# Performance work log

Hardware: AMD Instinct MI355X
Metric: run time of the kernel (lower is better)

## Reference

```python
import jax, jax.numpy as jnp
import numpy as np

TOP_K = 2

def setup_inputs() -> dict:
    key = jax.random.key(0)
    ks = jax.random.split(key, 8)
    B, T, C, E, I, S = 1, 2048, 2048, 8, 1408, 2816
    s = 0.02  # weight scale for numerical stability
    return {
        "x": jax.random.normal(ks[0], (B, T, C), jnp.float32),
        "gate_w": jax.random.normal(ks[1], (E, C), jnp.float32) * s,
        "w1": jax.random.normal(ks[2], (E, I, C), jnp.float32) * s,
        "w3": jax.random.normal(ks[3], (E, I, C), jnp.float32) * s,
        "w2": jax.random.normal(ks[4], (E, C, I), jnp.float32) * s,
        "sw1": jax.random.normal(ks[5], (S, C), jnp.float32) * s,
        "sw3": jax.random.normal(ks[6], (S, C), jnp.float32) * s,
        "sw2": jax.random.normal(ks[7], (C, S), jnp.float32) * s,
    }

def reference(x, gate_w, w1, w3, w2, sw1, sw3, sw2):
    B, T, C = x.shape
    E = gate_w.shape[0]
    xf = x.reshape(-1, C)                      # [N, C]
    N = xf.shape[0]
    # --- routing: top-k of raw logits, softmax over the k selected logits ---
    logits = xf @ gate_w.T                     # [N, E]
    pv, idx = jax.lax.top_k(logits, TOP_K)     # [N, K]
    pv = jax.nn.softmax(pv.astype(jnp.float32), axis=-1).astype(x.dtype)
    # token-expert combine weights (sum of probs per expert, scatter of top-k)
    tew = jnp.zeros((N, E), x.dtype).at[jnp.arange(N)[:, None], idx].add(pv)
    # --- experts (SwiGLU), computed densely over all experts and masked by tew ---
    h = jax.nn.silu(jnp.einsum('nc,eic->nei', xf, w1)) * jnp.einsum('nc,eic->nei', xf, w3)
    eo = jnp.einsum('nei,eci->nec', h, w2)     # [N, E, C]
    y = jnp.einsum('nec,ne->nc', eo, tew).reshape(B, T, C)
    # --- shared expert on the residual input ---
    sh = (jax.nn.silu(x @ sw1.T) * (x @ sw3.T)) @ sw2.T
    return y + sh
```

## Files before the change

kernel.cpp:

```cpp
#include <hip/hip_runtime.h>

#define DEVI __device__ __forceinline__

typedef __attribute__((ext_vector_type(4))) float f32x4;
typedef __attribute__((ext_vector_type(8))) short bf16x8;

static constexpr int NT = 2048;
static constexpr int CD = 2048;
static constexpr int NE = 8;
static constexpr int ID = 1408;
static constexpr int SD = 2816;
static constexpr int ROWS = 2 * NT;
static constexpr int ROWS_PAD = ROWS + 256;

DEVI unsigned short f2bf(float f) {
  unsigned u = __builtin_bit_cast(unsigned, f);
  u += 0x7fff + ((u >> 16) & 1);
  return (unsigned short)(u >> 16);
}
DEVI float bf2f(unsigned short s) { return __builtin_bit_cast(float, (unsigned)s << 16); }
DEVI float silu_f(float z) { return z / (1.f + __expf(-z)); }

DEVI void gll16(const void* g, void* l) {
  __builtin_amdgcn_global_load_lds((__attribute__((address_space(1))) void*)(void*)g,
                                   (__attribute__((address_space(3))) void*)l, 16, 0, 0);
}

DEVI void bar_sched() {
  __builtin_amdgcn_s_barrier();
  __builtin_amdgcn_sched_barrier(0);
}
DEVI void sched0() { __builtin_amdgcn_sched_barrier(0); }
DEVI void wait_vm0() { asm volatile("s_waitcnt vmcnt(0)" ::: "memory"); }
DEVI void wait_lgk0() { asm volatile("s_waitcnt lgkmcnt(0)" ::: "memory"); }

DEVI int swz8(int bid, int nwg) {
  constexpr int CH = 8, G = 64;
  int nfull = nwg - (nwg % G);
  if (bid >= nfull) return bid;
  int c = bid / G, r = bid % G;
  return c * G + (r % 8) * CH + (r / 8);
}

__global__ __launch_bounds__(256) void k_cvt(const float* __restrict__ s,
                                             unsigned short* __restrict__ d, int n8)
{
  int i = blockIdx.x * 256 + threadIdx.x;
  int stride = gridDim.x * 256;
  for (; i < n8; i += stride) {
    float4 a = ((const float4*)s)[2 * i];
    float4 b = ((const float4*)s)[2 * i + 1];
    ushort4 p0 = make_ushort4(f2bf(a.x), f2bf(a.y), f2bf(a.z), f2bf(a.w));
    ushort4 p1 = make_ushort4(f2bf(b.x), f2bf(b.y), f2bf(b.z), f2bf(b.w));
    ((ushort4*)d)[2 * i]     = p0;
    ((ushort4*)d)[2 * i + 1] = p1;
  }
}

__global__ __launch_bounds__(64) void k_router(const float* __restrict__ x,
    const float* __restrict__ gw, int* __restrict__ counts,
    int* __restrict__ eidx, int* __restrict__ posn, float* __restrict__ probs)
{
  const int n = blockIdx.x;
  const int lane = threadIdx.x;
  const float4* xr = (const float4*)(x + (size_t)n * CD);
  float acc[NE];
#pragma unroll
  for (int e = 0; e < NE; ++e) acc[e] = 0.f;
  for (int i = lane; i < CD / 4; i += 64) {
    float4 xv = xr[i];
#pragma unroll
    for (int e = 0; e < NE; ++e) {
      float4 gv = ((const float4*)(gw + (size_t)e * CD))[i];
      acc[e] += xv.x * gv.x + xv.y * gv.y + xv.z * gv.z + xv.w * gv.w;
    }
  }
#pragma unroll
  for (int e = 0; e < NE; ++e) {
    float v = acc[e];
#pragma unroll
    for (int off = 32; off > 0; off >>= 1) v += __shfl_down(v, off);
    acc[e] = v;
  }
  if (lane == 0) {
    int b0 = 0; float m0 = acc[0];
#pragma unroll
    for (int e = 1; e < NE; ++e) if (acc[e] > m0) { m0 = acc[e]; b0 = e; }
    int b1 = -1; float m1 = 0.f;
#pragma unroll
    for (int e = 0; e < NE; ++e) {
      if (e == b0) continue;
      if (b1 < 0 || acc[e] > m1) { m1 = acc[e]; b1 = e; }
    }
    float d = __expf(m1 - m0);
    float inv = 1.f / (1.f + d);
    eidx[2 * n] = b0; eidx[2 * n + 1] = b1;
    probs[2 * n] = inv; probs[2 * n + 1] = d * inv;
    posn[2 * n] = atomicAdd(&counts[b0], 1);
    posn[2 * n + 1] = atomicAdd(&counts[b1], 1);
  }
}

__global__ void k_scan(const int* __restrict__ counts, int* __restrict__ bases) {
  if (threadIdx.x == 0) {
    int s = 0;
    for (int e = 0; e < NE; ++e) { bases[e] = s; s += counts[e]; }
  }
}

__global__ __launch_bounds__(256) void k_build(const int* __restrict__ eidx,
    const int* __restrict__ posn, const int* __restrict__ bases,
    int* __restrict__ rows_of, int* __restrict__ row2tok)
{
  int n = blockIdx.x * 256 + threadIdx.x;
  if (n >= NT) return;
#pragma unroll
  for (int k = 0; k < 2; ++k) {
    int e = eidx[2 * n + k];
    int row = bases[e] + posn[2 * n + k];
    rows_of[2 * n + k] = row;
    row2tok[row] = n;
  }
}

__global__ __launch_bounds__(512, 2) void k_up(
    const unsigned short* __restrict__ xb,
    const unsigned short* __restrict__ w1b, const unsigned short* __restrict__ w3b,
    const unsigned short* __restrict__ sw1b, const unsigned short* __restrict__ sw3b,
    unsigned short* __restrict__ h, unsigned short* __restrict__ hs,
    const int* __restrict__ counts, const int* __restrict__ bases,
    const int* __restrict__ row2tok)
{
  extern __shared__ char sm[];
  constexpr int NSH = (NT / 256) * (SD / 128);
  constexpr int NWG = NSH + NE * (ID / 128) * (NT / 256);
  constexpr int NSTEP = CD / 64;

  int lin = swz8((int)blockIdx.x, NWG);
  int cls, mx, pn, e = 0;
  if (lin < NSH) { cls = 0; mx = lin % 8; pn = lin / 8; }
  else { cls = 1; int r = lin - NSH; mx = r % 8; r /= 8; pn = r % 11; e = r / 11; }

  int M = NT, baserow = 0;
  if (cls) { M = counts[e]; if (mx * 256 >= M) return; baserow = bases[e]; }
  const int m0 = mx * 256, n0 = pn * 128;

  const unsigned short* B1 = cls ? w1b + ((size_t)e * ID + n0) * CD : sw1b + (size_t)n0 * CD;
  const unsigned short* B3 = cls ? w3b + ((size_t)e * ID + n0) * CD : sw3b + (size_t)n0 * CD;

  const int tid = threadIdx.x, l = tid & 63, w = tid >> 6;
  const int wr = w >> 2, wn = w & 3;
  const int slot = ((tid & 7) ^ ((tid >> 3) & 7)) * 16;

  const char* aP[4];
#pragma unroll
  for (int t = 0; t < 4; ++t) {
    int r = t * 64 + (tid >> 3);
    const unsigned short* rb;
    if (cls) {
      int grow = m0 + r; int gr = grow < M ? grow : 0;
      rb = xb + (size_t)row2tok[baserow + gr] * CD;
    } else {
      rb = xb + (size_t)(m0 + r) * CD;
    }
    aP[t] = (const char*)rb + slot;
  }
  const char* bP1[2]; const char* bP3[2];
#pragma unroll
  for (int t = 0; t < 2; ++t) {
    int r = t * 64 + (tid >> 3);
    bP1[t] = (const char*)(B1 + (size_t)r * CD) + slot;
    bP3[t] = (const char*)(B3 + (size_t)r * CD) + slot;
  }

  f32x4 acc1[8][2], acc3[8][2];
#pragma unroll
  for (int m = 0; m < 8; ++m)
#pragma unroll
    for (int n = 0; n < 2; ++n) {
      acc1[m][n] = {0.f, 0.f, 0.f, 0.f};
      acc3[m][n] = {0.f, 0.f, 0.f, 0.f};
    }

  const int lrow = l & 15, lkg = l >> 4, l7 = l & 7;

  auto stage_first = [&](char* base, size_t kb) {
#pragma unroll
    for (int t = 0; t < 4; ++t) gll16(aP[t] + kb, base + t * 8192 + tid * 16);
  };
  auto stage_second = [&](char* base, size_t kb) {
    char* sB1 = base + 32768; char* sB3 = base + 49152;
#pragma unroll
    for (int t = 0; t < 2; ++t) {
      gll16(bP1[t] + kb, sB1 + t * 8192 + tid * 16);
      gll16(bP3[t] + kb, sB3 + t * 8192 + tid * 16);
    }
  };
  auto ldq = [&](bf16x8* fa, bf16x8* fb1, bf16x8* fb3, const char* cur, int mh, int kk) {
    const char* sA = cur; const char* sB1 = cur + 32768; const char* sB3 = cur + 49152;
    const int ao = ((kk * 4 + lkg) ^ l7) * 16;
#pragma unroll
    for (int m = 0; m < 4; ++m)
      fa[m] = *(const bf16x8*)(sA + (wr * 128 + mh * 64 + m * 16 + lrow) * 128 + ao);
#pragma unroll
    for (int n = 0; n < 2; ++n) {
      fb1[n] = *(const bf16x8*)(sB1 + (wn * 32 + n * 16 + lrow) * 128 + ao);
      fb3[n] = *(const bf16x8*)(sB3 + (wn * 32 + n * 16 + lrow) * 128 + ao);
    }
  };
  auto mmq = [&](const bf16x8* fa, const bf16x8* fb1, const bf16x8* fb3, int mh) {
    __builtin_amdgcn_s_setprio(1);
#pragma unroll
    for (int n = 0; n < 2; ++n)
#pragma unroll
      for (int m = 0; m < 4; ++m) {
        acc1[mh * 4 + m][n] = __builtin_amdgcn_mfma_f32_16x16x32_bf16(fa[m], fb1[n], acc1[mh * 4 + m][n], 0, 0, 0);
        acc3[mh * 4 + m][n] = __builtin_amdgcn_mfma_f32_16x16x32_bf16(fa[m], fb3[n], acc3[mh * 4 + m][n], 0, 0, 0);
      }
    __builtin_amdgcn_s_setprio(0);
  };

  stage_first(sm, 0);
  stage_second(sm, 0);
  wait_vm0(); bar_sched();

  bf16x8 Xa[4], Xb1[2], Xb3[2], Ya[4], Yb1[2], Yb3[2];

  for (int t = 0; t < NSTEP; ++t) {
    char* cur = sm + (size_t)(t & 1) * 65536;
    char* nxt = sm + (size_t)((t + 1) & 1) * 65536;
    size_t kb = (size_t)(t + 1) * 128;
    ldq(Xa, Xb1, Xb3, cur, 0, 0);
    sched0();
    if (t + 1 < NSTEP) stage_first(nxt, kb);
    ldq(Ya, Yb1, Yb3, cur, 1, 0);
    mmq(Xa, Xb1, Xb3, 0);
    sched0();
    if (t + 1 < NSTEP) stage_second(nxt, kb);
    ldq(Xa, Xb1, Xb3, cur, 0, 1);
    mmq(Ya, Yb1, Yb3, 1);
    sched0();
    ldq(Ya, Yb1, Yb3, cur, 1, 1);
    mmq(Xa, Xb1, Xb3, 0);
    sched0();
    mmq(Ya, Yb1, Yb3, 1);
    sched0();
    wait_vm0(); wait_lgk0();
    bar_sched();
  }

#pragma unroll
  for (int m = 0; m < 8; ++m) {
    int rb_ = m0 + wr * 128 + m * 16 + lkg * 4;
#pragma unroll
    for (int j = 0; j < 4; ++j) {
      int grow = rb_ + j;
      if (cls && grow >= M) continue;
#pragma unroll
      for (int n = 0; n < 2; ++n) {
        int gcol = n0 + wn * 32 + n * 16 + lrow;
        float hh = silu_f(acc1[m][n][j]) * acc3[m][n][j];
        if (cls) h[(size_t)(baserow + grow) * ID + gcol] = f2bf(hh);
        else     hs[(size_t)grow * SD + gcol] = f2bf(hh);
      }
    }
  }
}

__global__ __launch_bounds__(512, 2) void k_down(
    const unsigned short* __restrict__ h, const unsigned short* __restrict__ hs,
    const unsigned short* __restrict__ w2b, const unsigned short* __restrict__ sw2b,
    unsigned short* __restrict__ eo, float* __restrict__ y,
    const int* __restrict__ counts, const int* __restrict__ bases)
{
  extern __shared__ char sm[];
  constexpr int NRT = NE * (CD / 256) * (NT / 256);
  constexpr int NWG = NRT + (CD / 256) * (NT / 256);

  int lin = swz8((int)blockIdx.x, NWG);
  int cls, mx, pn, e = 0;
  if (lin < NRT) { cls = 1; mx = lin % 8; int r = lin / 8; pn = r % 8; e = r / 8; }
  else { cls = 0; int r = lin - NRT; mx = r % 8; pn = r / 8; }

  int M = NT, baserow = 0;
  if (cls) { M = counts[e]; if (mx * 256 >= M) return; baserow = bases[e]; }
  const int m0 = mx * 256, n0 = pn * 256;
  const int KD_ = cls ? ID : SD;
  const int nstep = KD_ / 64;

  const unsigned short* B = cls ? w2b + ((size_t)e * CD + n0) * ID : sw2b + (size_t)n0 * SD;

  const int tid = threadIdx.x, l = tid & 63, w = tid >> 6;
  const int wr = w >> 2, wn = w & 3;
  const int slot = ((tid & 7) ^ ((tid >> 3) & 7)) * 16;

  const char* aP[4]; const char* bP[4];
#pragma unroll
  for (int t = 0; t < 4; ++t) {
    int r = t * 64 + (tid >> 3);
    const unsigned short* rb = cls ? h + (size_t)(baserow + m0 + r) * ID
                                   : hs + (size_t)(m0 + r) * SD;
    aP[t] = (const char*)rb + slot;
    bP[t] = (const char*)(B + (size_t)r * KD_) + slot;
  }

  f32x4 acc[8][4];
#pragma unroll
  for (int m = 0; m < 8; ++m)
#pragma unroll
    for (int n = 0; n < 4; ++n) acc[m][n] = {0.f, 0.f, 0.f, 0.f};

  const int lrow = l & 15, lkg = l >> 4, l7 = l & 7;

  auto stage_first = [&](char* base, size_t kb) {
#pragma unroll
    for (int t = 0; t < 4; ++t) gll16(aP[t] + kb, base + t * 8192 + tid * 16);
  };
  auto stage_second = [&](char* base, size_t kb) {
    char* sB = base + 32768;
#pragma unroll
    for (int t = 0; t < 4; ++t) gll16(bP[t] + kb, sB + t * 8192 + tid * 16);
  };
  auto ldq = [&](bf16x8* fa, bf16x8* fb, const char* cur, int mh, int kk) {
    const char* sA = cur; const char* sB = cur + 32768;
    const int ao = ((kk * 4 + lkg) ^ l7) * 16;
#pragma unroll
    for (int m = 0; m < 4; ++m)
      fa[m] = *(const bf16x8*)(sA + (wr * 128 + mh * 64 + m * 16 + lrow) * 128 + ao);
#pragma unroll
    for (int n = 0; n < 4; ++n)
      fb[n] = *(const bf16x8*)(sB + (wn * 64 + n * 16 + lrow) * 128 + ao);
  };
  auto mmq = [&](const bf16x8* fa, const bf16x8* fb, int mh) {
    __builtin_amdgcn_s_setprio(1);
#pragma unroll
    for (int n = 0; n < 4; ++n)
#pragma unroll
      for (int m = 0; m < 4; ++m)
        acc[mh * 4 + m][n] = __builtin_amdgcn_mfma_f32_16x16x32_bf16(fa[m], fb[n], acc[mh * 4 + m][n], 0, 0, 0);
    __builtin_amdgcn_s_setprio(0);
  };

  stage_first(sm, 0);
  stage_second(sm, 0);
  wait_vm0(); bar_sched();

  bf16x8 Xa[4], Xb[4], Ya[4], Yb[4];

  for (int t = 0; t < nstep; ++t) {
    char* cur = sm + (size_t)(t & 1) * 65536;
    char* nxt = sm + (size_t)((t + 1) & 1) * 65536;
    size_t kb = (size_t)(t + 1) * 128;
    ldq(Xa, Xb, cur, 0, 0);
    sched0();
    if (t + 1 < nstep) stage_first(nxt, kb);
    ldq(Ya, Yb, cur, 1, 0);
    mmq(Xa, Xb, 0);
    sched0();
    if (t + 1 < nstep) stage_second(nxt, kb);
    ldq(Xa, Xb, cur, 0, 1);
    mmq(Ya, Yb, 1);
    sched0();
    ldq(Ya, Yb, cur, 1, 1);
    mmq(Xa, Xb, 0);
    sched0();
    mmq(Ya, Yb, 1);
    sched0();
    wait_vm0(); wait_lgk0();
    bar_sched();
  }

#pragma unroll
  for (int m = 0; m < 8; ++m) {
    int rb_ = m0 + wr * 128 + m * 16 + lkg * 4;
#pragma unroll
    for (int j = 0; j < 4; ++j) {
      int grow = rb_ + j;
      if (cls && grow >= M) continue;
#pragma unroll
      for (int n = 0; n < 4; ++n) {
        int gcol = n0 + wn * 64 + n * 16 + lrow;
        float v = acc[m][n][j];
        if (cls) eo[(size_t)(baserow + grow) * CD + gcol] = f2bf(v);
        else     y[(size_t)grow * CD + gcol] = v;
      }
    }
  }
}

__global__ __launch_bounds__(256) void k_combine(float* __restrict__ y,
    const unsigned short* __restrict__ eo, const int* __restrict__ rows_of,
    const float* __restrict__ probs)
{
  const int n = blockIdx.x;
  const int c = threadIdx.x * 8;
  const int r0 = rows_of[2 * n], r1 = rows_of[2 * n + 1];
  const float p0 = probs[2 * n], p1 = probs[2 * n + 1];
  bf16x8 e0 = *(const bf16x8*)(eo + (size_t)r0 * CD + c);
  bf16x8 e1 = *(const bf16x8*)(eo + (size_t)r1 * CD + c);
  float* yp = y + (size_t)n * CD + c;
  float4 y0 = *(float4*)yp, y1 = *(float4*)(yp + 4);
  y0.x += p0 * bf2f((unsigned short)e0[0]) + p1 * bf2f((unsigned short)e1[0]);
  y0.y += p0 * bf2f((unsigned short)e0[1]) + p1 * bf2f((unsigned short)e1[1]);
  y0.z += p0 * bf2f((unsigned short)e0[2]) + p1 * bf2f((unsigned short)e1[2]);
  y0.w += p0 * bf2f((unsigned short)e0[3]) + p1 * bf2f((unsigned short)e1[3]);
  y1.x += p0 * bf2f((unsigned short)e0[4]) + p1 * bf2f((unsigned short)e1[4]);
  y1.y += p0 * bf2f((unsigned short)e0[5]) + p1 * bf2f((unsigned short)e1[5]);
  y1.z += p0 * bf2f((unsigned short)e0[6]) + p1 * bf2f((unsigned short)e1[6]);
  y1.w += p0 * bf2f((unsigned short)e0[7]) + p1 * bf2f((unsigned short)e1[7]);
  *(float4*)yp = y0; *(float4*)(yp + 4) = y1;
}

extern "C" void kernel_launch(void* const* d_in, const int* in_sizes, int n_in,
                              void* d_out, int out_size, void* d_ws, size_t ws_size,
                              hipStream_t stream)
{
  const float* x   = (const float*)d_in[0];
  const float* gw  = (const float*)d_in[1];
  const float* w1  = (const float*)d_in[2];
  const float* w3  = (const float*)d_in[3];
  const float* w2  = (const float*)d_in[4];
  const float* sw1 = (const float*)d_in[5];
  const float* sw3 = (const float*)d_in[6];
  const float* sw2 = (const float*)d_in[7];
  float* y = (float*)d_out;

  char* p = (char*)d_ws;
  auto alloc = [&](size_t b) { char* r = p; p += (b + 255) & ~(size_t)255; return r; };
  int*   counts  = (int*)alloc(NE * 4);
  int*   bases   = (int*)alloc(NE * 4);
  int*   eidx    = (int*)alloc((size_t)NT * 2 * 4);
  int*   posn    = (int*)alloc((size_t)NT * 2 * 4);
  float* probs   = (float*)alloc((size_t)NT * 2 * 4);
  int*   rows_of = (int*)alloc((size_t)NT * 2 * 4);
  int*   row2tok = (int*)alloc((size_t)ROWS * 4);
  unsigned short* xb   = (unsigned short*)alloc((size_t)NT * CD * 2);
  unsigned short* w1b  = (unsigned short*)alloc((size_t)NE * ID * CD * 2);
  unsigned short* w3b  = (unsigned short*)alloc((size_t)NE * ID * CD * 2);
  unsigned short* w2b  = (unsigned short*)alloc((size_t)NE * CD * ID * 2);
  unsigned short* sw1b = (unsigned short*)alloc((size_t)SD * CD * 2);
  unsigned short* sw3b = (unsigned short*)alloc((size_t)SD * CD * 2);
  unsigned short* sw2b = (unsigned short*)alloc((size_t)CD * SD * 2);
  unsigned short* h    = (unsigned short*)alloc((size_t)ROWS_PAD * ID * 2);
  unsigned short* eo   = (unsigned short*)alloc((size_t)ROWS_PAD * CD * 2);
  unsigned short* hs   = (unsigned short*)alloc((size_t)NT * SD * 2);

  hipFuncSetAttribute((const void*)k_up,   hipFuncAttributeMaxDynamicSharedMemorySize, 131072);
  hipFuncSetAttribute((const void*)k_down, hipFuncAttributeMaxDynamicSharedMemorySize, 131072);

  hipMemsetAsync(counts, 0, NE * 4, stream);

  auto cvt = [&](const float* s, unsigned short* d, size_t n) {
    int n8 = (int)(n / 8);
    int grid = (n8 + 255) / 256; if (grid > 2048) grid = 2048;
    k_cvt<<<grid, 256, 0, stream>>>(s, d, n8);
  };
  cvt(x,   xb,   (size_t)NT * CD);
  cvt(w1,  w1b,  (size_t)NE * ID * CD);
  cvt(w3,  w3b,  (size_t)NE * ID * CD);
  cvt(w2,  w2b,  (size_t)NE * CD * ID);
  cvt(sw1, sw1b, (size_t)SD * CD);
  cvt(sw3, sw3b, (size_t)SD * CD);
  cvt(sw2, sw2b, (size_t)CD * SD);

  k_router<<<NT, 64, 0, stream>>>(x, gw, counts, eidx, posn, probs);
  k_scan<<<1, 64, 0, stream>>>(counts, bases);
  k_build<<<NT / 256, 256, 0, stream>>>(eidx, posn, bases, rows_of, row2tok);

  {
    constexpr int NWG = (NT / 256) * (SD / 128) + NE * (ID / 128) * (NT / 256);
    k_up<<<NWG, 512, 131072, stream>>>(xb, w1b, w3b, sw1b, sw3b, h, hs,
                                       counts, bases, row2tok);
  }
  {
    constexpr int NWG = NE * (CD / 256) * (NT / 256) + (CD / 256) * (NT / 256);
    k_down<<<NWG, 512, 131072, stream>>>(h, hs, w2b, sw2b, eo, y, counts, bases);
  }
  k_combine<<<NT, 256, 0, stream>>>(y, eo, rows_of, probs);
}
```

Baseline: 437.1 us.

## Shrink GEMM tiles and use triple-buffered LDS prefetch two steps ahead

```diff
diff --git a/kernel.cpp b/kernel.cpp
--- a/kernel.cpp
+++ b/kernel.cpp
@@ -12,6 +12,7 @@
 static constexpr int SD = 2816;
 static constexpr int ROWS = 2 * NT;
 static constexpr int ROWS_PAD = ROWS + 256;
+static constexpr int BUFSZ = 49152;
 
 DEVI unsigned short f2bf(float f) {
   unsigned u = __builtin_bit_cast(unsigned, f);
@@ -31,8 +32,8 @@
   __builtin_amdgcn_sched_barrier(0);
 }
 DEVI void sched0() { __builtin_amdgcn_sched_barrier(0); }
+DEVI void wait_vm6() { asm volatile("s_waitcnt vmcnt(6)" ::: "memory"); }
 DEVI void wait_vm0() { asm volatile("s_waitcnt vmcnt(0)" ::: "memory"); }
-DEVI void wait_lgk0() { asm volatile("s_waitcnt lgkmcnt(0)" ::: "memory"); }
 
 DEVI int swz8(int bid, int nwg) {
   constexpr int CH = 8, G = 64;
@@ -132,18 +133,18 @@
     const int* __restrict__ row2tok)
 {
   extern __shared__ char sm[];
-  constexpr int NSH = (NT / 256) * (SD / 128);
-  constexpr int NWG = NSH + NE * (ID / 128) * (NT / 256);
+  constexpr int NSH = (NT / 128) * (SD / 128);
+  constexpr int NWG = NSH + NE * (ID / 128) * (NT / 128);
   constexpr int NSTEP = CD / 64;
 
   int lin = swz8((int)blockIdx.x, NWG);
   int cls, mx, pn, e = 0;
-  if (lin < NSH) { cls = 0; mx = lin % 8; pn = lin / 8; }
-  else { cls = 1; int r = lin - NSH; mx = r % 8; r /= 8; pn = r % 11; e = r / 11; }
+  if (lin < NSH) { cls = 0; mx = lin % 16; pn = lin / 16; }
+  else { cls = 1; int r = lin - NSH; mx = r % 16; r /= 16; pn = r % 11; e = r / 11; }
 
   int M = NT, baserow = 0;
-  if (cls) { M = counts[e]; if (mx * 256 >= M) return; baserow = bases[e]; }
-  const int m0 = mx * 256, n0 = pn * 128;
+  if (cls) { M = counts[e]; if (mx * 128 >= M) return; baserow = bases[e]; }
+  const int m0 = mx * 128, n0 = pn * 128;
 
   const unsigned short* B1 = cls ? w1b + ((size_t)e * ID + n0) * CD : sw1b + (size_t)n0 * CD;
   const unsigned short* B3 = cls ? w3b + ((size_t)e * ID + n0) * CD : sw3b + (size_t)n0 * CD;
@@ -152,9 +153,9 @@
   const int wr = w >> 2, wn = w & 3;
   const int slot = ((tid & 7) ^ ((tid >> 3) & 7)) * 16;
 
-  const char* aP[4];
-#pragma unroll
-  for (int t = 0; t < 4; ++t) {
+  const char* aP[2];
+#pragma unroll
+  for (int t = 0; t < 2; ++t) {
     int r = t * 64 + (tid >> 3);
     const unsigned short* rb;
     if (cls) {
@@ -173,9 +174,9 @@
     bP3[t] = (const char*)(B3 + (size_t)r * CD) + slot;
   }
 
-  f32x4 acc1[8][2], acc3[8][2];
-#pragma unroll
-  for (int m = 0; m < 8; ++m)
+  f32x4 acc1[4][2], acc3[4][2];
+#pragma unroll
+  for (int m = 0; m < 4; ++m)
 #pragma unroll
     for (int n = 0; n < 2; ++n) {
       acc1[m][n] = {0.f, 0.f, 0.f, 0.f};
@@ -184,24 +185,24 @@
 
   const int lrow = l & 15, lkg = l >> 4, l7 = l & 7;
 
-  auto stage_first = [&](char* base, size_t kb) {
-#pragma unroll
-    for (int t = 0; t < 4; ++t) gll16(aP[t] + kb, base + t * 8192 + tid * 16);
-  };
-  auto stage_second = [&](char* base, size_t kb) {
-    char* sB1 = base + 32768; char* sB3 = base + 49152;
-#pragma unroll
-    for (int t = 0; t < 2; ++t) {
-      gll16(bP1[t] + kb, sB1 + t * 8192 + tid * 16);
-      gll16(bP3[t] + kb, sB3 + t * 8192 + tid * 16);
-    }
+  auto stageA = [&](char* buf, size_t kb) {
+    gll16(aP[0] + kb, buf + tid * 16);
+    gll16(aP[1] + kb, buf + 8192 + tid * 16);
+  };
+  auto stageB1c = [&](char* buf, size_t kb) {
+    gll16(bP1[0] + kb, buf + 16384 + tid * 16);
+    gll16(bP1[1] + kb, buf + 24576 + tid * 16);
+  };
+  auto stageB3c = [&](char* buf, size_t kb) {
+    gll16(bP3[0] + kb, buf + 32768 + tid * 16);
+    gll16(bP3[1] + kb, buf + 40960 + tid * 16);
   };
   auto ldq = [&](bf16x8* fa, bf16x8* fb1, bf16x8* fb3, const char* cur, int mh, int kk) {
-    const char* sA = cur; const char* sB1 = cur + 32768; const char* sB3 = cur + 49152;
+    const char* sA = cur; const char* sB1 = cur + 16384; const char* sB3 = cur + 32768;
     const int ao = ((kk * 4 + lkg) ^ l7) * 16;
 #pragma unroll
-    for (int m = 0; m < 4; ++m)
-      fa[m] = *(const bf16x8*)(sA + (wr * 128 + mh * 64 + m * 16 + lrow) * 128 + ao);
+    for (int m = 0; m < 2; ++m)
+      fa[m] = *(const bf16x8*)(sA + (wr * 64 + mh * 32 + m * 16 + lrow) * 128 + ao);
 #pragma unroll
     for (int n = 0; n < 2; ++n) {
       fb1[n] = *(const bf16x8*)(sB1 + (wn * 32 + n * 16 + lrow) * 128 + ao);
@@ -213,45 +214,46 @@
 #pragma unroll
     for (int n = 0; n < 2; ++n)
 #pragma unroll
-      for (int m = 0; m < 4; ++m) {
-        acc1[mh * 4 + m][n] = __builtin_amdgcn_mfma_f32_16x16x32_bf16(fa[m], fb1[n], acc1[mh * 4 + m][n], 0, 0, 0);
-        acc3[mh * 4 + m][n] = __builtin_amdgcn_mfma_f32_16x16x32_bf16(fa[m], fb3[n], acc3[mh * 4 + m][n], 0, 0, 0);
+      for (int m = 0; m < 2; ++m) {
+        acc1[mh * 2 + m][n] = __builtin_amdgcn_mfma_f32_16x16x32_bf16(fa[m], fb1[n], acc1[mh * 2 + m][n], 0, 0, 0);
+        acc3[mh * 2 + m][n] = __builtin_amdgcn_mfma_f32_16x16x32_bf16(fa[m], fb3[n], acc3[mh * 2 + m][n], 0, 0, 0);
       }
     __builtin_amdgcn_s_setprio(0);
   };
 
-  stage_first(sm, 0);
-  stage_second(sm, 0);
-  wait_vm0(); bar_sched();
-
-  bf16x8 Xa[4], Xb1[2], Xb3[2], Ya[4], Yb1[2], Yb3[2];
+  stageA(sm, 0); stageB1c(sm, 0); stageB3c(sm, 0);
+  stageA(sm + BUFSZ, 128); stageB1c(sm + BUFSZ, 128); stageB3c(sm + BUFSZ, 128);
+
+  bf16x8 Xa[2], Xb1[2], Xb3[2], Ya[2], Yb1[2], Yb3[2];
 
   for (int t = 0; t < NSTEP; ++t) {
-    char* cur = sm + (size_t)(t & 1) * 65536;
-    char* nxt = sm + (size_t)((t + 1) & 1) * 65536;
-    size_t kb = (size_t)(t + 1) * 128;
+    if (t == NSTEP - 1) wait_vm0(); else wait_vm6();
+    bar_sched();
+    const char* cur = sm + (size_t)(t % 3) * BUFSZ;
+    char* nb = sm + (size_t)((t + 2) % 3) * BUFSZ;
+    const bool pf = (t + 2 < NSTEP);
+    const size_t kb = (size_t)(t + 2) * 128;
     ldq(Xa, Xb1, Xb3, cur, 0, 0);
     sched0();
-    if (t + 1 < NSTEP) stage_first(nxt, kb);
+    if (pf) stageA(nb, kb);
     ldq(Ya, Yb1, Yb3, cur, 1, 0);
     mmq(Xa, Xb1, Xb3, 0);
     sched0();
-    if (t + 1 < NSTEP) stage_second(nxt, kb);
+    if (pf) stageB1c(nb, kb);
     ldq(Xa, Xb1, Xb3, cur, 0, 1);
     mmq(Ya, Yb1, Yb3, 1);
     sched0();
+    if (pf) stageB3c(nb, kb);
     ldq(Ya, Yb1, Yb3, cur, 1, 1);
     mmq(Xa, Xb1, Xb3, 0);
     sched0();
     mmq(Ya, Yb1, Yb3, 1);
     sched0();
-    wait_vm0(); wait_lgk0();
-    bar_sched();
-  }
-
-#pragma unroll
-  for (int m = 0; m < 8; ++m) {
-    int rb_ = m0 + wr * 128 + m * 16 + lkg * 4;
+  }
+
+#pragma unroll
+  for (int m = 0; m < 4; ++m) {
+    int rb_ = m0 + wr * 64 + m * 16 + lkg * 4;
 #pragma unroll
     for (int j = 0; j < 4; ++j) {
       int grow = rb_ + j;
@@ -274,17 +276,17 @@
     const int* __restrict__ counts, const int* __restrict__ bases)
 {
   extern __shared__ char sm[];
-  constexpr int NRT = NE * (CD / 256) * (NT / 256);
-  constexpr int NWG = NRT + (CD / 256) * (NT / 256);
+  constexpr int NRT = NE * (CD / 128) * (NT / 256);
+  constexpr int NWG = NRT + (CD / 128) * (NT / 256);
 
   int lin = swz8((int)blockIdx.x, NWG);
   int cls, mx, pn, e = 0;
-  if (lin < NRT) { cls = 1; mx = lin % 8; int r = lin / 8; pn = r % 8; e = r / 8; }
+  if (lin < NRT) { cls = 1; mx = lin % 8; int r = lin / 8; pn = r % 16; e = r / 16; }
   else { cls = 0; int r = lin - NRT; mx = r % 8; pn = r / 8; }
 
   int M = NT, baserow = 0;
   if (cls) { M = counts[e]; if (mx * 256 >= M) return; baserow = bases[e]; }
-  const int m0 = mx * 256, n0 = pn * 256;
+  const int m0 = mx * 256, n0 = pn * 128;
   const int KD_ = cls ? ID : SD;
   const int nstep = KD_ / 64;
 
@@ -294,32 +296,39 @@
   const int wr = w >> 2, wn = w & 3;
   const int slot = ((tid & 7) ^ ((tid >> 3) & 7)) * 16;
 
-  const char* aP[4]; const char* bP[4];
+  const char* aP[4]; const char* bP[2];
 #pragma unroll
   for (int t = 0; t < 4; ++t) {
     int r = t * 64 + (tid >> 3);
     const unsigned short* rb = cls ? h + (size_t)(baserow + m0 + r) * ID
                                    : hs + (size_t)(m0 + r) * SD;
     aP[t] = (const char*)rb + slot;
+  }
+#pragma unroll
+  for (int t = 0; t < 2; ++t) {
+    int r = t * 64 + (tid >> 3);
     bP[t] = (const char*)(B + (size_t)r * KD_) + slot;
   }
 
-  f32x4 acc[8][4];
+  f32x4 acc[8][2];
 #pragma unroll
   for (int m = 0; m < 8; ++m)
 #pragma unroll
-    for (int n = 0; n < 4; ++n) acc[m][n] = {0.f, 0.f, 0.f, 0.f};
+    for (int n = 0; n < 2; ++n) acc[m][n] = {0.f, 0.f, 0.f, 0.f};
 
   const int lrow = l & 15, lkg = l >> 4, l7 = l & 7;
 
-  auto stage_first = [&](char* base, size_t kb) {
-#pragma unroll
-    for (int t = 0; t < 4; ++t) gll16(aP[t] + kb, base + t * 8192 + tid * 16);
-  };
-  auto stage_second = [&](char* base, size_t kb) {
-    char* sB = base + 32768;
-#pragma unroll
-    for (int t = 0; t < 4; ++t) gll16(bP[t] + kb, sB + t * 8192 + tid * 16);
+  auto stageA01 = [&](char* buf, size_t kb) {
+    gll16(aP[0] + kb, buf + tid * 16);
+    gll16(aP[1] + kb, buf + 8192 + tid * 16);
+  };
+  auto stageA23 = [&](char* buf, size_t kb) {
+    gll16(aP[2] + kb, buf + 16384 + tid * 16);
+    gll16(aP[3] + kb, buf + 24576 + tid * 16);
+  };
+  auto stageB = [&](char* buf, size_t kb) {
+    gll16(bP[0] + kb, buf + 32768 + tid * 16);
+    gll16(bP[1] + kb, buf + 40960 + tid * 16);
   };
   auto ldq = [&](bf16x8* fa, bf16x8* fb, const char* cur, int mh, int kk) {
     const char* sA = cur; const char* sB = cur + 32768;
@@ -328,46 +337,47 @@
     for (int m = 0; m < 4; ++m)
       fa[m] = *(const bf16x8*)(sA + (wr * 128 + mh * 64 + m * 16 + lrow) * 128 + ao);
 #pragma unroll
-    for (int n = 0; n < 4; ++n)
-      fb[n] = *(const bf16x8*)(sB + (wn * 64 + n * 16 + lrow) * 128 + ao);
+    for (int n = 0; n < 2; ++n)
+      fb[n] = *(const bf16x8*)(sB + (wn * 32 + n * 16 + lrow) * 128 + ao);
   };
   auto mmq = [&](const bf16x8* fa, const bf16x8* fb, int mh) {
     __builtin_amdgcn_s_setprio(1);
 #pragma unroll
-    for (int n = 0; n < 4; ++n)
+    for (int n = 0; n < 2; ++n)
 #pragma unroll
       for (int m = 0; m < 4; ++m)
         acc[mh * 4 + m][n] = __builtin_amdgcn_mfma_f32_16x16x32_bf16(fa[m], fb[n], acc[mh * 4 + m][n], 0, 0, 0);
     __builtin_amdgcn_s_setprio(0);
   };
 
-  stage_first(sm, 0);
-  stage_second(sm, 0);
-  wait_vm0(); bar_sched();
-
-  bf16x8 Xa[4], Xb[4], Ya[4], Yb[4];
+  stageA01(sm, 0); stageA23(sm, 0); stageB(sm, 0);
+  stageA01(sm + BUFSZ, 128); stageA23(sm + BUFSZ, 128); stageB(sm + BUFSZ, 128);
+
+  bf16x8 Xa[4], Xb[2], Ya[4], Yb[2];
 
   for (int t = 0; t < nstep; ++t) {
-    char* cur = sm + (size_t)(t & 1) * 65536;
-    char* nxt = sm + (size_t)((t + 1) & 1) * 65536;
-    size_t kb = (size_t)(t + 1) * 128;
+    if (t == nstep - 1) wait_vm0(); else wait_vm6();
+    bar_sched();
+    const char* cur = sm + (size_t)(t % 3) * BUFSZ;
+    char* nb = sm + (size_t)((t + 2) % 3) * BUFSZ;
+    const bool pf = (t + 2 < nstep);
+    const size_t kb = (size_t)(t + 2) * 128;
     ldq(Xa, Xb, cur, 0, 0);
     sched0();
-    if (t + 1 < nstep) stage_first(nxt, kb);
+    if (pf) stageA01(nb, kb);
     ldq(Ya, Yb, cur, 1, 0);
     mmq(Xa, Xb, 0);
     sched0();
-    if (t + 1 < nstep) stage_second(nxt, kb);
+    if (pf) stageA23(nb, kb);
     ldq(Xa, Xb, cur, 0, 1);
     mmq(Ya, Yb, 1);
     sched0();
+    if (pf) stageB(nb, kb);
     ldq(Ya, Yb, cur, 1, 1);
     mmq(Xa, Xb, 0);
     sched0();
     mmq(Ya, Yb, 1);
     sched0();
-    wait_vm0(); wait_lgk0();
-    bar_sched();
   }
 
 #pragma unroll
@@ -378,8 +388,8 @@
       int grow = rb_ + j;
       if (cls && grow >= M) continue;
 #pragma unroll
-      for (int n = 0; n < 4; ++n) {
-        int gcol = n0 + wn * 64 + n * 16 + lrow;
+      for (int n = 0; n < 2; ++n) {
+        int gcol = n0 + wn * 32 + n * 16 + lrow;
         float v = acc[m][n][j];
         if (cls) eo[(size_t)(baserow + grow) * CD + gcol] = f2bf(v);
         else     y[(size_t)grow * CD + gcol] = v;
@@ -445,8 +455,8 @@
   unsigned short* eo   = (unsigned short*)alloc((size_t)ROWS_PAD * CD * 2);
   unsigned short* hs   = (unsigned short*)alloc((size_t)NT * SD * 2);
 
-  hipFuncSetAttribute((const void*)k_up,   hipFuncAttributeMaxDynamicSharedMemorySize, 131072);
-  hipFuncSetAttribute((const void*)k_down, hipFuncAttributeMaxDynamicSharedMemorySize, 131072);
+  hipFuncSetAttribute((const void*)k_up,   hipFuncAttributeMaxDynamicSharedMemorySize, 3 * BUFSZ);
+  hipFuncSetAttribute((const void*)k_down, hipFuncAttributeMaxDynamicSharedMemorySize, 3 * BUFSZ);
 
   hipMemsetAsync(counts, 0, NE * 4, stream);
 
@@ -468,13 +478,13 @@
   k_build<<<NT / 256, 256, 0, stream>>>(eidx, posn, bases, rows_of, row2tok);
 
   {
-    constexpr int NWG = (NT / 256) * (SD / 128) + NE * (ID / 128) * (NT / 256);
-    k_up<<<NWG, 512, 131072, stream>>>(xb, w1b, w3b, sw1b, sw3b, h, hs,
-                                       counts, bases, row2tok);
+    constexpr int NWG = (NT / 128) * (SD / 128) + NE * (ID / 128) * (NT / 128);
+    k_up<<<NWG, 512, 3 * BUFSZ, stream>>>(xb, w1b, w3b, sw1b, sw3b, h, hs,
+                                          counts, bases, row2tok);
   }
   {
-    constexpr int NWG = NE * (CD / 256) * (NT / 256) + (CD / 256) * (NT / 256);
-    k_down<<<NWG, 512, 131072, stream>>>(h, hs, w2b, sw2b, eo, y, counts, bases);
+    constexpr int NWG = NE * (CD / 128) * (NT / 256) + (CD / 128) * (NT / 256);
+    k_down<<<NWG, 512, 3 * BUFSZ, stream>>>(h, hs, w2b, sw2b, eo, y, counts, bases);
   }
   k_combine<<<NT, 256, 0, stream>>>(y, eo, rows_of, probs);
 }
```

After: 451.1 us. +3.2%, slower.

## Fuse fp32-to-bf16 weight conversion into GEMM B-tile staging

Applied to the files above, without the earlier changes.

```diff
diff --git a/kernel.cpp b/kernel.cpp
--- a/kernel.cpp
+++ b/kernel.cpp
@@ -34,6 +34,13 @@
 DEVI void wait_vm0() { asm volatile("s_waitcnt vmcnt(0)" ::: "memory"); }
 DEVI void wait_lgk0() { asm volatile("s_waitcnt lgkmcnt(0)" ::: "memory"); }
 
+DEVI void pack8(const float4& a, const float4& b, void* dst) {
+  ushort4 p0 = make_ushort4(f2bf(a.x), f2bf(a.y), f2bf(a.z), f2bf(a.w));
+  ushort4 p1 = make_ushort4(f2bf(b.x), f2bf(b.y), f2bf(b.z), f2bf(b.w));
+  ((ushort4*)dst)[0] = p0;
+  ((ushort4*)dst)[1] = p1;
+}
+
 DEVI int swz8(int bid, int nwg) {
   constexpr int CH = 8, G = 64;
   int nfull = nwg - (nwg % G);
@@ -50,10 +57,7 @@
   for (; i < n8; i += stride) {
     float4 a = ((const float4*)s)[2 * i];
     float4 b = ((const float4*)s)[2 * i + 1];
-    ushort4 p0 = make_ushort4(f2bf(a.x), f2bf(a.y), f2bf(a.z), f2bf(a.w));
-    ushort4 p1 = make_ushort4(f2bf(b.x), f2bf(b.y), f2bf(b.z), f2bf(b.w));
-    ((ushort4*)d)[2 * i]     = p0;
-    ((ushort4*)d)[2 * i + 1] = p1;
+    pack8(a, b, (ushort4*)d + 2 * i);
   }
 }
 
@@ -125,8 +129,8 @@
 
 __global__ __launch_bounds__(512, 2) void k_up(
     const unsigned short* __restrict__ xb,
-    const unsigned short* __restrict__ w1b, const unsigned short* __restrict__ w3b,
-    const unsigned short* __restrict__ sw1b, const unsigned short* __restrict__ sw3b,
+    const float* __restrict__ w1, const float* __restrict__ w3,
+    const float* __restrict__ sw1, const float* __restrict__ sw3,
     unsigned short* __restrict__ h, unsigned short* __restrict__ hs,
     const int* __restrict__ counts, const int* __restrict__ bases,
     const int* __restrict__ row2tok)
@@ -145,12 +149,12 @@
   if (cls) { M = counts[e]; if (mx * 256 >= M) return; baserow = bases[e]; }
   const int m0 = mx * 256, n0 = pn * 128;
 
-  const unsigned short* B1 = cls ? w1b + ((size_t)e * ID + n0) * CD : sw1b + (size_t)n0 * CD;
-  const unsigned short* B3 = cls ? w3b + ((size_t)e * ID + n0) * CD : sw3b + (size_t)n0 * CD;
+  const float* B1f = cls ? w1 + ((size_t)e * ID + n0) * CD : sw1 + (size_t)n0 * CD;
+  const float* B3f = cls ? w3 + ((size_t)e * ID + n0) * CD : sw3 + (size_t)n0 * CD;
 
   const int tid = threadIdx.x, l = tid & 63, w = tid >> 6;
   const int wr = w >> 2, wn = w & 3;
-  const int slot = ((tid & 7) ^ ((tid >> 3) & 7)) * 16;
+  const int sg = (tid & 7) ^ ((tid >> 3) & 7);
 
   const char* aP[4];
 #pragma unroll
@@ -163,14 +167,14 @@
     } else {
       rb = xb + (size_t)(m0 + r) * CD;
     }
-    aP[t] = (const char*)rb + slot;
-  }
-  const char* bP1[2]; const char* bP3[2];
+    aP[t] = (const char*)rb + sg * 16;
+  }
+  const float* bP1[2]; const float* bP3[2];
 #pragma unroll
   for (int t = 0; t < 2; ++t) {
     int r = t * 64 + (tid >> 3);
-    bP1[t] = (const char*)(B1 + (size_t)r * CD) + slot;
-    bP3[t] = (const char*)(B3 + (size_t)r * CD) + slot;
+    bP1[t] = B1f + (size_t)r * CD + sg * 8;
+    bP3[t] = B3f + (size_t)r * CD + sg * 8;
   }
 
   f32x4 acc1[8][2], acc3[8][2];
@@ -184,16 +188,25 @@
 
   const int lrow = l & 15, lkg = l >> 4, l7 = l & 7;
 
-  auto stage_first = [&](char* base, size_t kb) {
+  auto stageA = [&](char* base, size_t kb) {
 #pragma unroll
     for (int t = 0; t < 4; ++t) gll16(aP[t] + kb, base + t * 8192 + tid * 16);
   };
-  auto stage_second = [&](char* base, size_t kb) {
+  auto issueB = [&](float4* r1, float4* r3, int k0) {
+#pragma unroll
+    for (int t = 0; t < 2; ++t) {
+      r1[2 * t]     = *(const float4*)(bP1[t] + k0);
+      r1[2 * t + 1] = *(const float4*)(bP1[t] + k0 + 4);
+      r3[2 * t]     = *(const float4*)(bP3[t] + k0);
+      r3[2 * t + 1] = *(const float4*)(bP3[t] + k0 + 4);
+    }
+  };
+  auto writeB = [&](char* base, const float4* r1, const float4* r3) {
     char* sB1 = base + 32768; char* sB3 = base + 49152;
 #pragma unroll
     for (int t = 0; t < 2; ++t) {
-      gll16(bP1[t] + kb, sB1 + t * 8192 + tid * 16);
-      gll16(bP3[t] + kb, sB3 + t * 8192 + tid * 16);
+      pack8(r1[2 * t], r1[2 * t + 1], sB1 + t * 8192 + tid * 16);
+      pack8(r3[2 * t], r3[2 * t + 1], sB3 + t * 8192 + tid * 16);
     }
   };
   auto ldq = [&](bf16x8* fa, bf16x8* fb1, bf16x8* fb3, const char* cur, int mh, int kk) {
@@ -220,29 +233,36 @@
     __builtin_amdgcn_s_setprio(0);
   };
 
-  stage_first(sm, 0);
-  stage_second(sm, 0);
-  wait_vm0(); bar_sched();
+  {
+    float4 r1[4], r3[4];
+    issueB(r1, r3, 0);
+    stageA(sm, 0);
+    writeB(sm, r1, r3);
+    wait_vm0(); wait_lgk0(); bar_sched();
+  }
 
   bf16x8 Xa[4], Xb1[2], Xb3[2], Ya[4], Yb1[2], Yb3[2];
 
   for (int t = 0; t < NSTEP; ++t) {
     char* cur = sm + (size_t)(t & 1) * 65536;
     char* nxt = sm + (size_t)((t + 1) & 1) * 65536;
-    size_t kb = (size_t)(t + 1) * 128;
+    const bool pf = (t + 1 < NSTEP);
+    const size_t kb = (size_t)(t + 1) * 128;
+    float4 r1[4], r3[4];
     ldq(Xa, Xb1, Xb3, cur, 0, 0);
     sched0();
-    if (t + 1 < NSTEP) stage_first(nxt, kb);
+    if (pf) issueB(r1, r3, (t + 1) * 64);
     ldq(Ya, Yb1, Yb3, cur, 1, 0);
     mmq(Xa, Xb1, Xb3, 0);
     sched0();
-    if (t + 1 < NSTEP) stage_second(nxt, kb);
+    if (pf) stageA(nxt, kb);
     ldq(Xa, Xb1, Xb3, cur, 0, 1);
     mmq(Ya, Yb1, Yb3, 1);
     sched0();
     ldq(Ya, Yb1, Yb3, cur, 1, 1);
     mmq(Xa, Xb1, Xb3, 0);
     sched0();
+    if (pf) writeB(nxt, r1, r3);
     mmq(Ya, Yb1, Yb3, 1);
     sched0();
     wait_vm0(); wait_lgk0();
@@ -269,7 +289,7 @@
 
 __global__ __launch_bounds__(512, 2) void k_down(
     const unsigned short* __restrict__ h, const unsigned short* __restrict__ hs,
-    const unsigned short* __restrict__ w2b, const unsigned short* __restrict__ sw2b,
+    const float* __restrict__ w2, const float* __restrict__ sw2,
     unsigned short* __restrict__ eo, float* __restrict__ y,
     const int* __restrict__ counts, const int* __restrict__ bases)
 {
@@ -288,20 +308,20 @@
   const int KD_ = cls ? ID : SD;
   const int nstep = KD_ / 64;
 
-  const unsigned short* B = cls ? w2b + ((size_t)e * CD + n0) * ID : sw2b + (size_t)n0 * SD;
+  const float* Bf = cls ? w2 + ((size_t)e * CD + n0) * ID : sw2 + (size_t)n0 * SD;
 
   const int tid = threadIdx.x, l = tid & 63, w = tid >> 6;
   const int wr = w >> 2, wn = w & 3;
-  const int slot = ((tid & 7) ^ ((tid >> 3) & 7)) * 16;
-
-  const char* aP[4]; const char* bP[4];
+  const int sg = (tid & 7) ^ ((tid >> 3) & 7);
+
+  const char* aP[4]; const float* bP[4];
 #pragma unroll
   for (int t = 0; t < 4; ++t) {
     int r = t * 64 + (tid >> 3);
     const unsigned short* rb = cls ? h + (size_t)(baserow + m0 + r) * ID
                                    : hs + (size_t)(m0 + r) * SD;
-    aP[t] = (const char*)rb + slot;
-    bP[t] = (const char*)(B + (size_t)r * KD_) + slot;
+    aP[t] = (const char*)rb + sg * 16;
+    bP[t] = Bf + (size_t)r * KD_ + sg * 8;
   }
 
   f32x4 acc[8][4];
@@ -312,14 +332,22 @@
 
   const int lrow = l & 15, lkg = l >> 4, l7 = l & 7;
 
-  auto stage_first = [&](char* base, size_t kb) {
+  auto stageA = [&](char* base, size_t kb) {
 #pragma unroll
     for (int t = 0; t < 4; ++t) gll16(aP[t] + kb, base + t * 8192 + tid * 16);
   };
-  auto stage_second = [&](char* base, size_t kb) {
+  auto issueB = [&](float4* r, int k0) {
+#pragma unroll
+    for (int t = 0; t < 4; ++t) {
+      r[2 * t]     = *(const float4*)(bP[t] + k0);
+      r[2 * t + 1] = *(const float4*)(bP[t] + k0 + 4);
+    }
+  };
+  auto writeB = [&](char* base, const float4* r) {
     char* sB = base + 32768;
 #pragma unroll
-    for (int t = 0; t < 4; ++t) gll16(bP[t] + kb, sB + t * 8192 + tid * 16);
+    for (int t = 0; t < 4; ++t)
+      pack8(r[2 * t], r[2 * t + 1], sB + t * 8192 + tid * 16);
   };
   auto ldq = [&](bf16x8* fa, bf16x8* fb, const char* cur, int mh, int kk) {
     const char* sA = cur; const char* sB = cur + 32768;
@@ -341,29 +369,36 @@
     __builtin_amdgcn_s_setprio(0);
   };
 
-  stage_first(sm, 0);
-  stage_second(sm, 0);
-  wait_vm0(); bar_sched();
+  {
+    float4 r[8];
+    issueB(r, 0);
+    stageA(sm, 0);
+    writeB(sm, r);
+    wait_vm0(); wait_lgk0(); bar_sched();
+  }
 
   bf16x8 Xa[4], Xb[4], Ya[4], Yb[4];
 
   for (int t = 0; t < nstep; ++t) {
     char* cur = sm + (size_t)(t & 1) * 65536;
     char* nxt = sm + (size_t)((t + 1) & 1) * 65536;
-    size_t kb = (size_t)(t + 1) * 128;
+    const bool pf = (t + 1 < nstep);
+    const size_t kb = (size_t)(t + 1) * 128;
+    float4 r[8];
     ldq(Xa, Xb, cur, 0, 0);
     sched0();
-    if (t + 1 < nstep) stage_first(nxt, kb);
+    if (pf) issueB(r, (t + 1) * 64);
     ldq(Ya, Yb, cur, 1, 0);
     mmq(Xa, Xb, 0);
     sched0();
-    if (t + 1 < nstep) stage_second(nxt, kb);
+    if (pf) stageA(nxt, kb);
     ldq(Xa, Xb, cur, 0, 1);
     mmq(Ya, Yb, 1);
     sched0();
     ldq(Ya, Yb, cur, 1, 1);
     mmq(Xa, Xb, 0);
     sched0();
+    if (pf) writeB(nxt, r);
     mmq(Ya, Yb, 1);
     sched0();
     wait_vm0(); wait_lgk0();
@@ -434,34 +469,21 @@
   float* probs   = (float*)alloc((size_t)NT * 2 * 4);
   int*   rows_of = (int*)alloc((size_t)NT * 2 * 4);
   int*   row2tok = (int*)alloc((size_t)ROWS * 4);
-  unsigned short* xb   = (unsigned short*)alloc((size_t)NT * CD * 2);
-  unsigned short* w1b  = (unsigned short*)alloc((size_t)NE * ID * CD * 2);
-  unsigned short* w3b  = (unsigned short*)alloc((size_t)NE * ID * CD * 2);
-  unsigned short* w2b  = (unsigned short*)alloc((size_t)NE * CD * ID * 2);
-  unsigned short* sw1b = (unsigned short*)alloc((size_t)SD * CD * 2);
-  unsigned short* sw3b = (unsigned short*)alloc((size_t)SD * CD * 2);
-  unsigned short* sw2b = (unsigned short*)alloc((size_t)CD * SD * 2);
-  unsigned short* h    = (unsigned short*)alloc((size_t)ROWS_PAD * ID * 2);
-  unsigned short* eo   = (unsigned short*)alloc((size_t)ROWS_PAD * CD * 2);
-  unsigned short* hs   = (unsigned short*)alloc((size_t)NT * SD * 2);
+  unsigned short* xb = (unsigned short*)alloc((size_t)NT * CD * 2);
+  unsigned short* h  = (unsigned short*)alloc((size_t)ROWS_PAD * ID * 2);
+  unsigned short* eo = (unsigned short*)alloc((size_t)ROWS_PAD * CD * 2);
+  unsigned short* hs = (unsigned short*)alloc((size_t)NT * SD * 2);
 
   hipFuncSetAttribute((const void*)k_up,   hipFuncAttributeMaxDynamicSharedMemorySize, 131072);
   hipFuncSetAttribute((const void*)k_down, hipFuncAttributeMaxDynamicSharedMemorySize, 131072);
 
   hipMemsetAsync(counts, 0, NE * 4, stream);
 
-  auto cvt = [&](const float* s, unsigned short* d, size_t n) {
-    int n8 = (int)(n / 8);
+  {
+    int n8 = (int)((size_t)NT * CD / 8);
     int grid = (n8 + 255) / 256; if (grid > 2048) grid = 2048;
-    k_cvt<<<grid, 256, 0, stream>>>(s, d, n8);
-  };
-  cvt(x,   xb,   (size_t)NT * CD);
-  cvt(w1,  w1b,  (size_t)NE * ID * CD);
-  cvt(w3,  w3b,  (size_t)NE * ID * CD);
-  cvt(w2,  w2b,  (size_t)NE * CD * ID);
-  cvt(sw1, sw1b, (size_t)SD * CD);
-  cvt(sw3, sw3b, (size_t)SD * CD);
-  cvt(sw2, sw2b, (size_t)CD * SD);
+    k_cvt<<<grid, 256, 0, stream>>>(x, xb, n8);
+  }
 
   k_router<<<NT, 64, 0, stream>>>(x, gw, counts, eidx, posn, probs);
   k_scan<<<1, 64, 0, stream>>>(counts, bases);
@@ -469,12 +491,12 @@
 
   {
     constexpr int NWG = (NT / 256) * (SD / 128) + NE * (ID / 128) * (NT / 256);
-    k_up<<<NWG, 512, 131072, stream>>>(xb, w1b, w3b, sw1b, sw3b, h, hs,
+    k_up<<<NWG, 512, 131072, stream>>>(xb, w1, w3, sw1, sw3, h, hs,
                                        counts, bases, row2tok);
   }
   {
     constexpr int NWG = NE * (CD / 256) * (NT / 256) + (CD / 256) * (NT / 256);
-    k_down<<<NWG, 512, 131072, stream>>>(h, hs, w2b, sw2b, eo, y, counts, bases);
+    k_down<<<NWG, 512, 131072, stream>>>(h, hs, w2, sw2, eo, y, counts, bases);
   }
   k_combine<<<NT, 256, 0, stream>>>(y, eo, rows_of, probs);
 }
```

Measured after the change: 537.8 us. +23.0%, slower.
